# Optimization experiments

Measured on AMD Instinct MI355X. Metric: run time of the kernel, lower is better.

## Reference

```python
import jax, jax.numpy as jnp
import numpy as np

FEAT_STRIDE = 16
PRE_NMS_TOPN = 6000
POST_NMS_TOPN = 300
NMS_THRESH = 0.7
NEG = -1e9  # sentinel for suppressed scores


def generate_anchors(base_size=16, ratios=np.array([0.5, 1.0, 2.0]), scales=np.array([8.0, 16.0, 32.0])):
    ctr = (base_size - 1) / 2.0
    size = float(base_size * base_size)
    ws_r = np.round(np.sqrt(size / ratios))
    hs_r = np.round(ws_r * ratios)
    ws = (ws_r[:, None] * scales[None, :]).reshape(-1)
    hs = (hs_r[:, None] * scales[None, :]).reshape(-1)
    return np.stack([ctr - 0.5 * (ws - 1), ctr - 0.5 * (hs - 1),
                     ctr + 0.5 * (ws - 1), ctr + 0.5 * (hs - 1)], axis=1).astype(np.float32)

ANCHORS = jnp.asarray(generate_anchors())  # [A, 4]


def bbox_transform_inv(anchors, deltas):
    # anchors [N,4], deltas [B,N,4] -> [B,N,4]
    w = anchors[:, 2] - anchors[:, 0] + 1.0
    h = anchors[:, 3] - anchors[:, 1] + 1.0
    cx = anchors[:, 0] + 0.5 * w
    cy = anchors[:, 1] + 0.5 * h
    dx, dy, dw, dh = deltas[..., 0], deltas[..., 1], deltas[..., 2], deltas[..., 3]
    pcx = dx * w + cx
    pcy = dy * h + cy
    pw = jnp.exp(dw) * w
    ph = jnp.exp(dh) * h
    return jnp.stack([pcx - 0.5 * pw, pcy - 0.5 * ph, pcx + 0.5 * pw, pcy + 0.5 * ph], axis=-1)


def nms_single(boxes, scores):
    # Greedy NMS on pre-sorted candidates; boxes [N,4], scores [N].
    areas = (boxes[:, 2] - boxes[:, 0] + 1.0) * (boxes[:, 3] - boxes[:, 1] + 1.0)

    def body(sc, _):
        i = jnp.argmax(sc)
        valid = sc[i] > NEG / 2
        b = boxes[i]
        xx1 = jnp.maximum(b[0], boxes[:, 0])
        yy1 = jnp.maximum(b[1], boxes[:, 1])
        xx2 = jnp.minimum(b[2], boxes[:, 2])
        yy2 = jnp.minimum(b[3], boxes[:, 3])
        inter = jnp.maximum(xx2 - xx1 + 1.0, 0.0) * jnp.maximum(yy2 - yy1 + 1.0, 0.0)
        iou = inter / (areas[i] + areas - inter)
        sc = jnp.where(iou > NMS_THRESH, NEG, sc)  # suppress (includes self, iou=1)
        return sc, (i, valid)

    _, (keep, valid) = jax.lax.scan(body, scores, None, length=POST_NMS_TOPN)
    kept_boxes = jnp.where(valid[:, None], boxes[keep], 0.0)  # pad rows -> zeros
    return kept_boxes


def reference(scores, bbox_deltas, im_info):
    B, _, H, W = scores.shape
    A = ANCHORS.shape[0]
    # fg probs: second set of A channels -> [B, K*A]
    fg = jnp.transpose(scores[:, A:, :, :], (0, 2, 3, 1)).reshape(B, -1)
    deltas = jnp.transpose(bbox_deltas, (0, 2, 3, 1)).reshape(B, -1, 4)

    # Shifted anchors over the feature grid: [K*A, 4]
    sx = jnp.arange(W, dtype=jnp.float32) * FEAT_STRIDE
    sy = jnp.arange(H, dtype=jnp.float32) * FEAT_STRIDE
    mx, my = jnp.meshgrid(sx, sy)  # [H, W]
    shifts = jnp.stack([mx.ravel(), my.ravel(), mx.ravel(), my.ravel()], axis=1)  # [K,4]
    anchors = (ANCHORS[None, :, :] + shifts[:, None, :]).reshape(-1, 4)

    proposals = bbox_transform_inv(anchors, deltas)  # [B, K*A, 4]

    # Clip to image per batch element (im_info = [height, width, scale])
    wmax = (im_info[:, 1] - 1.0)[:, None]
    hmax = (im_info[:, 0] - 1.0)[:, None]
    proposals = jnp.stack([
        jnp.clip(proposals[..., 0], 0.0, wmax),
        jnp.clip(proposals[..., 1], 0.0, hmax),
        jnp.clip(proposals[..., 2], 0.0, wmax),
        jnp.clip(proposals[..., 3], 0.0, hmax)], axis=-1)

    # Top pre_nms_topN by score (sorted descending)
    top_scores, top_idx = jax.lax.top_k(fg, PRE_NMS_TOPN)            # [B, pre]
    top_boxes = jnp.take_along_axis(proposals, top_idx[..., None], axis=1)  # [B, pre, 4]

    kept = jax.vmap(nms_single)(top_boxes, top_scores)  # [B, post, 4]

    batch_col = jnp.broadcast_to(
        jnp.arange(B, dtype=kept.dtype)[:, None, None], (B, POST_NMS_TOPN, 1))
    return jnp.concatenate([batch_col, kept], axis=-1)  # [B, post, 5]


def setup_inputs() -> dict:
    key = jax.random.key(0)
    k1, k2 = jax.random.split(key)
    B, A, H, W = 16, 9, 192, 192
    scores = jax.random.uniform(k1, (B, 2 * A, H, W), dtype=jnp.float32)
    bbox_deltas = jax.random.normal(k2, (B, 4 * A, H, W), dtype=jnp.float32) * 0.5
    im_info = jnp.tile(jnp.array([[H * 16.0, W * 16.0, 1.0]], dtype=jnp.float32), (B, 1))
    return {"scores": scores, "bbox_deltas": bbox_deltas, "im_info": im_info}
```

## Files before the change

### kernel.cpp

```cpp
#include <hip/hip_runtime.h>
#include <stdint.h>

#define A_NUM    9
#define W_FEAT   192
#define H_FEAT   192
#define K_FEAT   (W_FEAT * H_FEAT)
#define N_ANCH   (K_FEAT * A_NUM)
#define BATCH    16
#define PRE_NMS  6000
#define POST_NMS 300
#define CAP      8192
#define CHUNK    4096
#define BPB      (N_ANCH / CHUNK)
#define CPA      (K_FEAT / CHUNK)
#define SORT2    2048
#define NWORD    (SORT2 / 64)
#define SLOTS    64

#define T2KEY    0xBF7Fu

typedef unsigned long long u64;

__constant__ float c_anchors[A_NUM][4] = {
    { -84.f,  -40.f,  99.f,  55.f},
    {-176.f,  -88.f, 191.f, 103.f},
    {-360.f, -184.f, 375.f, 199.f},
    { -56.f,  -56.f,  71.f,  71.f},
    {-120.f, -120.f, 135.f, 135.f},
    {-248.f, -248.f, 263.f, 263.f},
    { -36.f,  -80.f,  51.f,  95.f},
    { -80.f, -168.f,  95.f, 183.f},
    {-168.f, -344.f, 183.f, 359.f},
};

__device__ __forceinline__ unsigned key_bits(float s) {
    unsigned ub = __float_as_uint(s);
    return (ub & 0x80000000u) ? ~ub : (ub | 0x80000000u);
}

__device__ __forceinline__ const float* chunk_ptr(const float* scores, int blk,
                                                  int& b, int& a, int& koff) {
    b = blk / BPB;
    int chunk = blk - b * BPB;
    a = chunk / CPA;
    koff = (chunk - a * CPA) * CHUNK;
    return scores + ((size_t)(b * 2 * A_NUM + A_NUM + a)) * K_FEAT + koff;
}

__device__ __forceinline__ void hist_add(unsigned* lh, unsigned bin) {
    unsigned long long peers = __ballot(1);
    #pragma unroll
    for (int bit = 0; bit < 8; ++bit) {
        unsigned long long vote = __ballot((bin >> bit) & 1);
        peers &= ((bin >> bit) & 1) ? vote : ~vote;
    }
    int lane = threadIdx.x & 63;
    if (lane == (int)(__ffsll((long long)peers) - 1))
        atomicAdd(&lh[bin], (unsigned)__popcll(peers));
}

__device__ __forceinline__ float4 decode_box(unsigned n, const float* __restrict__ deltas,
                                             int b, float wmax, float hmax) {
    unsigned kk = n / A_NUM, a = n - kk * A_NUM;
    unsigned hh = kk / W_FEAT, ww = kk - hh * W_FEAT;
    size_t dbase = ((size_t)(b * 4 * A_NUM + 4 * a)) * K_FEAT + kk;
    float dx = deltas[dbase];
    float dy = deltas[dbase + (size_t)K_FEAT];
    float dw = deltas[dbase + (size_t)2 * K_FEAT];
    float dh = deltas[dbase + (size_t)3 * K_FEAT];
    float ax1 = c_anchors[a][0] + ww * 16.0f;
    float ay1 = c_anchors[a][1] + hh * 16.0f;
    float ax2 = c_anchors[a][2] + ww * 16.0f;
    float ay2 = c_anchors[a][3] + hh * 16.0f;
    float waf = ax2 - ax1 + 1.0f, haf = ay2 - ay1 + 1.0f;
    float cx = ax1 + 0.5f * waf, cy = ay1 + 0.5f * haf;
    float pcx = dx * waf + cx, pcy = dy * haf + cy;
    float pw = expf(dw) * waf, ph = expf(dh) * haf;
    float4 box;
    box.x = fminf(fmaxf(pcx - 0.5f * pw, 0.f), wmax);
    box.y = fminf(fmaxf(pcy - 0.5f * ph, 0.f), hmax);
    box.z = fminf(fmaxf(pcx + 0.5f * pw, 0.f), wmax);
    box.w = fminf(fmaxf(pcy + 0.5f * ph, 0.f), hmax);
    return box;
}

__device__ __forceinline__ bool iou_over(float4 a, float aa, float4 c, float ca) {
    float xx1 = fmaxf(a.x, c.x), yy1 = fmaxf(a.y, c.y);
    float xx2 = fminf(a.z, c.z), yy2 = fminf(a.w, c.w);
    float iw = fmaxf(xx2 - xx1 + 1.f, 0.f);
    float ih = fmaxf(yy2 - yy1 + 1.f, 0.f);
    float inter = iw * ih;
    return inter > 0.7f * (aa + ca - inter);
}

__device__ __forceinline__ u64 shflxor64(u64 v, int j) {
    unsigned lo = (unsigned)v, hi = (unsigned)(v >> 32);
    lo = __shfl_xor(lo, j, 64);
    hi = __shfl_xor(hi, j, 64);
    return ((u64)hi << 32) | lo;
}

__global__ __launch_bounds__(256) void compact_kernel(
        const float* __restrict__ scores,
        unsigned* __restrict__ cnt_blk,
        u64* __restrict__ cand) {
    __shared__ u64 sbuf[256];
    __shared__ unsigned scount;
    int tid = threadIdx.x;
    if (tid == 0) scount = 0;
    __syncthreads();
    int b, a, koff;
    const float* p = chunk_ptr(scores, blockIdx.x, b, a, koff);
    const float4* p4 = (const float4*)p;
    #pragma unroll
    for (int it = 0; it < CHUNK / 1024; ++it) {
        float4 v = p4[it * 256 + tid];
        unsigned e0 = (unsigned)(koff + (it * 256 + tid) * 4);
        float vv[4] = {v.x, v.y, v.z, v.w};
        #pragma unroll
        for (int j = 0; j < 4; ++j) {
            unsigned ub = key_bits(vv[j]);
            if ((ub >> 16) >= T2KEY) {
                unsigned n = (e0 + j) * A_NUM + a;
                unsigned pos = atomicAdd(&scount, 1u);
                if (pos < 256)
                    sbuf[pos] = ((u64)ub << 32) | (unsigned)(~n);
            }
        }
    }
    __syncthreads();
    unsigned c = scount;
    if (tid == 0) cnt_blk[blockIdx.x] = c;
    unsigned cw = c < SLOTS ? c : SLOTS;
    if (tid < cw) cand[(size_t)blockIdx.x * SLOTS + tid] = sbuf[tid];
}

#define KEYRD(I)  ((((u64)khi[(I)]) << 32) | klo[(I)])
#define KEYWR(I, V) do { khi[(I)] = (unsigned)((V) >> 32); klo[(I)] = (unsigned)(V); } while (0)

#define CE_SHFL(E, J, DESC) do { \
    u64 _v = shflxor64((E), (J)); \
    bool _kmax = ((DESC) == ((l & (J)) == 0)); \
    (E) = _kmax ? ((E) > _v ? (E) : _v) : ((E) < _v ? (E) : _v); \
} while (0)

#define CE_PAIR(A, B, DESC) do { \
    u64 _mx = (A) > (B) ? (A) : (B); \
    u64 _mn = (A) > (B) ? (B) : (A); \
    if (DESC) { (A) = _mx; (B) = _mn; } else { (A) = _mn; (B) = _mx; } \
} while (0)

#define LDS_PHASE(K, J) do { \
    _Pragma("unroll") \
    for (int pp = 0; pp < 2; ++pp) { \
        unsigned p = (unsigned)tid + (unsigned)pp * 512u; \
        unsigned i = ((p & ~((unsigned)(J) - 1u)) << 1) | (p & ((unsigned)(J) - 1u)); \
        unsigned ixj = i | (unsigned)(J); \
        u64 x = KEYRD(i), y = KEYRD(ixj); \
        bool dsc = ((i & (unsigned)(K)) == 0u); \
        if (dsc ? (x < y) : (x > y)) { KEYWR(i, y); KEYWR(ixj, x); } \
    } \
    __syncthreads(); \
} while (0)

#define REG_TAIL(D) do { \
    int seg = w << 8; \
    bool d = (D); \
    u64 e0 = KEYRD(seg + l); \
    u64 e1 = KEYRD(seg + 64 + l); \
    u64 e2 = KEYRD(seg + 128 + l); \
    u64 e3 = KEYRD(seg + 192 + l); \
    CE_PAIR(e0, e2, d); CE_PAIR(e1, e3, d); \
    CE_PAIR(e0, e1, d); CE_PAIR(e2, e3, d); \
    _Pragma("unroll") \
    for (int j = 32; j >= 1; j >>= 1) { \
        CE_SHFL(e0, j, d); CE_SHFL(e1, j, d); \
        CE_SHFL(e2, j, d); CE_SHFL(e3, j, d); \
    } \
    KEYWR(seg + l, e0); KEYWR(seg + 64 + l, e1); \
    KEYWR(seg + 128 + l, e2); KEYWR(seg + 192 + l, e3); \
    __syncthreads(); \
} while (0)

__global__ __launch_bounds__(512) void sort_kernel(
        const unsigned* __restrict__ cnt_blk,
        const u64* __restrict__ cand,
        const float* __restrict__ deltas,
        const float* __restrict__ im_info,
        float4* __restrict__ bxg,
        unsigned* __restrict__ m2arr,
        unsigned* __restrict__ okarr) {
    int b = blockIdx.x;
    __shared__ unsigned khi[SORT2];
    __shared__ unsigned klo[SORT2];
    __shared__ unsigned offs[BPB + 1];
    __shared__ unsigned ovfl;
    int tid = threadIdx.x;
    int l = tid & 63, w = tid >> 6;

    if (tid == 0) { ovfl = 0; offs[0] = 0; }
    __syncthreads();
    if (tid < BPB) {
        unsigned c = cnt_blk[b * BPB + tid];
        if (c > SLOTS) atomicOr(&ovfl, 1u);
        offs[tid + 1] = (c > SLOTS) ? SLOTS : c;
    }
    for (int i = tid; i < SORT2; i += 512) { khi[i] = 0u; klo[i] = 0u; }
    __syncthreads();
    if (tid == 0)
        for (int i = 1; i <= BPB; ++i) offs[i] += offs[i - 1];
    __syncthreads();
    unsigned m2 = offs[BPB];
    bool ok = (!ovfl) && (m2 >= 1) && (m2 <= SORT2);

    if (ok) {
        for (int s = w; s < BPB; s += 8) {
            unsigned c = offs[s + 1] - offs[s];
            if ((unsigned)l < c) {
                u64 k = cand[(size_t)(b * BPB + s) * SLOTS + l];
                KEYWR(offs[s] + l, k);
            }
        }
    }
    __syncthreads();

    if (ok) {
        {
            int seg = w << 8;
            u64 e0 = KEYRD(seg + l);
            u64 e1 = KEYRD(seg + 64 + l);
            u64 e2 = KEYRD(seg + 128 + l);
            u64 e3 = KEYRD(seg + 192 + l);
            #pragma unroll
            for (int k = 2; k <= 32; k <<= 1) {
                bool d = ((l & k) == 0);
                #pragma unroll
                for (int j = k >> 1; j >= 1; j >>= 1) {
                    CE_SHFL(e0, j, d); CE_SHFL(e1, j, d);
                    CE_SHFL(e2, j, d); CE_SHFL(e3, j, d);
                }
            }
            #pragma unroll
            for (int j = 32; j >= 1; j >>= 1) {
                CE_SHFL(e0, j, true);  CE_SHFL(e1, j, false);
                CE_SHFL(e2, j, true);  CE_SHFL(e3, j, false);
            }
            CE_PAIR(e0, e1, true); CE_PAIR(e2, e3, false);
            #pragma unroll
            for (int j = 32; j >= 1; j >>= 1) {
                CE_SHFL(e0, j, true);  CE_SHFL(e1, j, true);
                CE_SHFL(e2, j, false); CE_SHFL(e3, j, false);
            }
            {
                bool d = ((w & 1) == 0);
                CE_PAIR(e0, e2, d); CE_PAIR(e1, e3, d);
                CE_PAIR(e0, e1, d); CE_PAIR(e2, e3, d);
                #pragma unroll
                for (int j = 32; j >= 1; j >>= 1) {
                    CE_SHFL(e0, j, d); CE_SHFL(e1, j, d);
                    CE_SHFL(e2, j, d); CE_SHFL(e3, j, d);
                }
            }
            KEYWR(seg + l, e0); KEYWR(seg + 64 + l, e1);
            KEYWR(seg + 128 + l, e2); KEYWR(seg + 192 + l, e3);
        }
        __syncthreads();
        LDS_PHASE(512, 256);                 REG_TAIL(((w & 2) == 0));
        LDS_PHASE(1024, 512); LDS_PHASE(1024, 256);  REG_TAIL(((w & 4) == 0));
        LDS_PHASE(2048, 1024); LDS_PHASE(2048, 512); LDS_PHASE(2048, 256);
        REG_TAIL(true);

        float wmax = im_info[b * 3 + 1] - 1.0f;
        float hmax = im_info[b * 3 + 0] - 1.0f;
        int mceil = (int)((m2 + 63u) & ~63u);
        for (int i = tid; i < mceil; i += 512) {
            float4 v;
            if (i < (int)m2) v = decode_box(~klo[i], deltas, b, wmax, hmax);
            else             v = make_float4(-3e9f, -3e9f, -3e9f, -3e9f);
            bxg[(size_t)b * SORT2 + i] = v;
        }
    }
    if (tid == 0) { m2arr[b] = m2; okarr[b] = ok ? 1u : 0u; }
}

__global__ __launch_bounds__(256) void mask_kernel(
        const float4* __restrict__ bxg,
        const unsigned* __restrict__ m2arr,
        const unsigned* __restrict__ okarr,
        u64* __restrict__ mask) {
    int b = blockIdx.x >> 5;
    int t = blockIdx.x & 31;
    if (!okarr[b]) return;
    unsigned m2 = m2arr[b];
    if ((unsigned)(t * 64) >= m2) return;
    __shared__ float4 sb[SORT2];
    __shared__ float  sa[SORT2];
    int tid = threadIdx.x;
    int mceil = (int)((m2 + 63u) & ~63u);
    for (int i = tid; i < mceil; i += 256) {
        float4 v = bxg[(size_t)b * SORT2 + i];
        sb[i] = v;
        sa[i] = (v.z - v.x + 1.f) * (v.w - v.y + 1.f);
    }
    __syncthreads();
    int r = t * 64 + (tid >> 2);
    int q = tid & 3;
    float4 rb = sb[r];
    float  ra = sa[r];
    u64* mrow = mask + ((size_t)b * SORT2 + r) * NWORD;
    for (int w = t + q; w < NWORD; w += 4) {
        if (w * 64 >= mceil) break;
        u64 bits = 0;
        #pragma unroll 4
        for (int jj = 0; jj < 64; ++jj) {
            int j = w * 64 + jj;
            bits |= ((u64)(iou_over(rb, ra, sb[j], sa[j]) ? 1 : 0)) << jj;
        }
        mrow[w] = bits;
    }
}

__global__ __launch_bounds__(512) void resolve_fb_kernel(
        const float4* __restrict__ bxg,
        const u64* __restrict__ mask,
        const unsigned* __restrict__ m2arr,
        const unsigned* __restrict__ okarr,
        const float* __restrict__ scores,
        const float* __restrict__ deltas,
        const float* __restrict__ im_info,
        float4* __restrict__ fbbox,
        float* __restrict__ out) {
    int b = blockIdx.x;
    int tid = threadIdx.x;
    __shared__ unsigned short kept_idx[POST_NMS];
    __shared__ unsigned nk_sh;
    __shared__ unsigned lh[256];
    __shared__ unsigned d8_sh, above_sh, tbin_sh, fbcnt;
    __shared__ u64 keys[CAP];

    bool okb = (okarr[b] != 0);
    if (tid == 0) nk_sh = 0;
    __syncthreads();

    if (okb && tid < 64) {
        int lane = tid;
        int m2 = (int)m2arr[b];
        const u64* mb = mask + (size_t)b * SORT2 * NWORD;
        u64 S = 0;
        int w32 = lane & 31;
        bool hiHalf = lane >= 32;
        int nchunks = (m2 + 63) >> 6;
        u64 dpre = mb[(size_t)lane * NWORD + 0];
        int nk = 0;
        for (int c = 0; c < nchunks && nk < POST_NMS; ++c) {
            int base = c * 64;
            int nvalid = min(64, m2 - base);
            u64 d = dpre;
            if (c + 1 < nchunks)
                dpre = mb[(size_t)(base + 64 + lane) * NWORD + (c + 1)];
            unsigned wl0 = __builtin_amdgcn_readlane((unsigned)S, c);
            unsigned wh0 = __builtin_amdgcn_readlane((unsigned)(S >> 32), c);
            unsigned wl1 = __builtin_amdgcn_readlane((unsigned)S, c + 32);
            unsigned wh1 = __builtin_amdgcn_readlane((unsigned)(S >> 32), c + 32);
            u64 Sc = (((u64)wh0 << 32) | wl0) | (((u64)wh1 << 32) | wl1);
            u64 live = ~Sc;
            if (nvalid < 64) live &= (1ull << nvalid) - 1ull;
            u64 keptC = 0;
            while (live && nk < POST_NMS) {
                int il = (int)__ffsll((long long)live) - 1;
                unsigned dlo = __builtin_amdgcn_readlane((unsigned)d, il);
                unsigned dhi = __builtin_amdgcn_readlane((unsigned)(d >> 32), il);
                u64 drow = ((u64)dhi << 32) | dlo;
                live &= ~drow;
                live &= ~(1ull << il);
                if (lane == 0) kept_idx[nk] = (unsigned short)(base + il);
                keptC |= 1ull << il;
                ++nk;
            }
            if (nk < POST_NMS && c + 1 < nchunks && keptC) {
                long long kc = (long long)keptC;
                while (kc) {
                    int r0  = (int)__ffsll(kc) - 1; kc &= kc - 1;
                    int r1  = (int)__ffsll(kc) - 1; kc &= kc - 1;
                    int r2  = (int)__ffsll(kc) - 1; kc &= kc - 1;
                    int r3  = (int)__ffsll(kc) - 1; kc &= kc - 1;
                    int r4  = (int)__ffsll(kc) - 1; kc &= kc - 1;
                    int r5  = (int)__ffsll(kc) - 1; kc &= kc - 1;
                    int r6  = (int)__ffsll(kc) - 1; kc &= kc - 1;
                    int r7  = (int)__ffsll(kc) - 1; kc &= kc - 1;
                    int r8  = (int)__ffsll(kc) - 1; kc &= kc - 1;
                    int r9  = (int)__ffsll(kc) - 1; kc &= kc - 1;
                    int r10 = (int)__ffsll(kc) - 1; kc &= kc - 1;
                    int r11 = (int)__ffsll(kc) - 1; kc &= kc - 1;
                    int r12 = (int)__ffsll(kc) - 1; kc &= kc - 1;
                    int r13 = (int)__ffsll(kc) - 1; kc &= kc - 1;
                    int r14 = (int)__ffsll(kc) - 1; kc &= kc - 1;
                    int r15 = (int)__ffsll(kc) - 1; kc &= kc - 1;
                    int s0 = hiHalf ? r1  : r0;
                    int s1 = hiHalf ? r3  : r2;
                    int s2 = hiHalf ? r5  : r4;
                    int s3 = hiHalf ? r7  : r6;
                    int s4 = hiHalf ? r9  : r8;
                    int s5 = hiHalf ? r11 : r10;
                    int s6 = hiHalf ? r13 : r12;
                    int s7 = hiHalf ? r15 : r14;
                    u64 a0 = 0, a1 = 0, a2 = 0, a3 = 0;
                    u64 a4 = 0, a5 = 0, a6 = 0, a7 = 0;
                    if (s0 >= 0) a0 = mb[(size_t)(base + s0) * NWORD + w32];
                    if (s1 >= 0) a1 = mb[(size_t)(base + s1) * NWORD + w32];
                    if (s2 >= 0) a2 = mb[(size_t)(base + s2) * NWORD + w32];
                    if (s3 >= 0) a3 = mb[(size_t)(base + s3) * NWORD + w32];
                    if (s4 >= 0) a4 = mb[(size_t)(base + s4) * NWORD + w32];
                    if (s5 >= 0) a5 = mb[(size_t)(base + s5) * NWORD + w32];
                    if (s6 >= 0) a6 = mb[(size_t)(base + s6) * NWORD + w32];
                    if (s7 >= 0) a7 = mb[(size_t)(base + s7) * NWORD + w32];
                    S |= (a0 | a1) | (a2 | a3) | (a4 | a5) | (a6 | a7);
                }
            }
        }
        if (lane == 0) nk_sh = (unsigned)nk;
    }
    __syncthreads();

    unsigned nk = nk_sh;
    bool ok_final = okb && (nk == POST_NMS);
    if (ok_final) {
        const float4* bx = bxg + (size_t)b * SORT2;
        for (int t = tid; t < POST_NMS; t += 512) {
            float4 kb = bx[kept_idx[t]];
            float* o = out + ((size_t)b * POST_NMS + t) * 5;
            o[0] = (float)b;
            o[1] = kb.x; o[2] = kb.y; o[3] = kb.z; o[4] = kb.w;
        }
        return;
    }

    if (tid < 256) lh[tid] = 0;
    __syncthreads();
    for (int a = 0; a < A_NUM; ++a) {
        const float* p = scores + ((size_t)(b * 2 * A_NUM + A_NUM + a)) * K_FEAT;
        for (int k = tid; k < K_FEAT; k += 512)
            hist_add(lh, key_bits(p[k]) >> 24);
    }
    __syncthreads();
    if (tid == 0) {
        unsigned acc = 0; int d = 0;
        for (int i = 255; i >= 0; --i) {
            unsigned v = lh[i];
            if (acc + v >= PRE_NMS) { d = i; break; }
            acc += v;
        }
        d8_sh = (unsigned)d; above_sh = acc;
    }
    __syncthreads();
    unsigned dd = d8_sh;
    if (tid < 256) lh[tid] = 0;
    __syncthreads();
    for (int a = 0; a < A_NUM; ++a) {
        const float* p = scores + ((size_t)(b * 2 * A_NUM + A_NUM + a)) * K_FEAT;
        for (int k = tid; k < K_FEAT; k += 512) {
            unsigned u = key_bits(p[k]);
            if ((u >> 24) == dd) hist_add(lh, (u >> 16) & 0xFF);
        }
    }
    __syncthreads();
    if (tid == 0) {
        unsigned acc = above_sh; int d = 0;
        for (int i = 255; i >= 0; --i) {
            unsigned v = lh[i];
            if (acc + v >= PRE_NMS) { d = i; break; }
            acc += v;
        }
        tbin_sh = (dd << 8) | (unsigned)d;
        fbcnt = 0;
    }
    __syncthreads();
    unsigned tb = tbin_sh;
    for (int i = tid; i < CAP; i += 512) keys[i] = 0ULL;
    __syncthreads();
    for (int a = 0; a < A_NUM; ++a) {
        const float* p = scores + ((size_t)(b * 2 * A_NUM + A_NUM + a)) * K_FEAT;
        for (int k = tid; k < K_FEAT; k += 512) {
            unsigned u = key_bits(p[k]);
            if ((u >> 16) >= tb) {
                unsigned n = (unsigned)k * A_NUM + (unsigned)a;
                unsigned pos = atomicAdd(&fbcnt, 1u);
                if (pos < CAP) keys[pos] = ((u64)u << 32) | (unsigned)(~n);
            }
        }
    }
    __syncthreads();
    for (unsigned k = 2; k <= CAP; k <<= 1) {
        for (unsigned j = k >> 1; j > 0; j >>= 1) {
            #pragma unroll
            for (int pp = 0; pp < 8; ++pp) {
                unsigned p = (unsigned)tid + (unsigned)pp * 512u;
                unsigned i = ((p & ~(j - 1)) << 1) | (p & (j - 1));
                unsigned ixj = i | j;
                u64 x = keys[i], y = keys[ixj];
                bool desc = ((i & k) == 0);
                if (desc ? (x < y) : (x > y)) { keys[i] = y; keys[ixj] = x; }
            }
            __syncthreads();
        }
    }
    float wmax = im_info[b * 3 + 1] - 1.0f;
    float hmax = im_info[b * 3 + 0] - 1.0f;
    for (int i = tid; i < PRE_NMS; i += 512) {
        unsigned n = ~(unsigned)(keys[i] & 0xFFFFFFFFull);
        float4 box = make_float4(0.f, 0.f, 0.f, 0.f);
        if (n < N_ANCH) box = decode_box(n, deltas, b, wmax, hmax);
        fbbox[(size_t)b * PRE_NMS + i] = box;
    }
    __syncthreads();
    if (tid >= 64) return;
    int lane = tid;
    float4 k0, k1v, k2v, k3v, k4v;
    float a0 = 1.f, a1 = 1.f, a2 = 1.f, a3 = 1.f, a4 = 1.f;
    k0 = k1v = k2v = k3v = k4v = make_float4(0.f, 0.f, 0.f, 0.f);
    const float4* bb = fbbox + (size_t)b * PRE_NMS;
    int nk2 = 0;
    for (int i = 0; i < PRE_NMS && nk2 < POST_NMS; ++i) {
        float4 cur = bb[i];
        float ca = (cur.z - cur.x + 1.f) * (cur.w - cur.y + 1.f);
        bool s = false;
        if (nk2 > 0)   { bool v = lane < nk2;       s |= v && iou_over(k0,  a0, cur, ca); }
        if (nk2 > 64)  { bool v = 64 + lane < nk2;  s |= v && iou_over(k1v, a1, cur, ca); }
        if (nk2 > 128) { bool v = 128 + lane < nk2; s |= v && iou_over(k2v, a2, cur, ca); }
        if (nk2 > 192) { bool v = 192 + lane < nk2; s |= v && iou_over(k3v, a3, cur, ca); }
        if (nk2 > 256) { bool v = 256 + lane < nk2; s |= v && iou_over(k4v, a4, cur, ca); }
        if (!__any(s)) {
            int r = nk2 >> 6;
            if (lane == (nk2 & 63)) {
                if      (r == 0) { k0  = cur; a0 = ca; }
                else if (r == 1) { k1v = cur; a1 = ca; }
                else if (r == 2) { k2v = cur; a2 = ca; }
                else if (r == 3) { k3v = cur; a3 = ca; }
                else             { k4v = cur; a4 = ca; }
            }
            if (lane == 0) {
                float* o = out + ((size_t)b * POST_NMS + nk2) * 5;
                o[0] = (float)b;
                o[1] = cur.x; o[2] = cur.y; o[3] = cur.z; o[4] = cur.w;
            }
            ++nk2;
        }
    }
    for (int t = nk2 + lane; t < POST_NMS; t += 64) {
        float* o = out + ((size_t)b * POST_NMS + t) * 5;
        o[0] = (float)b;
        o[1] = 0.f; o[2] = 0.f; o[3] = 0.f; o[4] = 0.f;
    }
}

extern "C" void kernel_launch(void* const* d_in, const int* in_sizes, int n_in,
                              void* d_out, int out_size, void* d_ws, size_t ws_size,
                              hipStream_t stream) {
    const float* scores  = (const float*)d_in[0];
    const float* deltas  = (const float*)d_in[1];
    const float* im_info = (const float*)d_in[2];
    float* out = (float*)d_out;

    size_t off = 0;
    unsigned* cnt_blk = (unsigned*)((char*)d_ws + off);
    off += (size_t)BATCH * BPB * 4;
    off = (off + 255) & ~(size_t)255;
    u64* cand = (u64*)((char*)d_ws + off);
    off += (size_t)BATCH * BPB * SLOTS * 8;
    off = (off + 255) & ~(size_t)255;
    unsigned* m2arr = (unsigned*)((char*)d_ws + off);
    off += (size_t)BATCH * 4;
    off = (off + 255) & ~(size_t)255;
    unsigned* okarr = (unsigned*)((char*)d_ws + off);
    off += (size_t)BATCH * 4;
    off = (off + 255) & ~(size_t)255;
    float4* bxg = (float4*)((char*)d_ws + off);
    off += (size_t)BATCH * SORT2 * 16;
    off = (off + 255) & ~(size_t)255;
    u64* mask = (u64*)((char*)d_ws + off);
    off += (size_t)BATCH * SORT2 * NWORD * 8;
    off = (off + 255) & ~(size_t)255;
    float4* fbbox = (float4*)((char*)d_ws + off);

    compact_kernel   <<<BATCH * BPB, 256, 0, stream>>>(scores, cnt_blk, cand);
    sort_kernel      <<<BATCH, 512, 0, stream>>>(cnt_blk, cand, deltas, im_info,
                                                 bxg, m2arr, okarr);
    mask_kernel      <<<BATCH * 32, 256, 0, stream>>>(bxg, m2arr, okarr, mask);
    resolve_fb_kernel<<<BATCH, 512, 0, stream>>>(bxg, mask, m2arr, okarr,
                                                 scores, deltas, im_info,
                                                 fbbox, out);
}
```

Baseline: 105.9 us.

## Double-buffer NMS mask chunks in LDS with producer waves prefetching

The serial greedy NMS resolve now stages each 64-row chunk of the suppression mask in shared memory. Waves 1-7 prefetch the next chunk into a second buffer while wave 0 scans the current chunk, and all waves synchronize once per chunk. This replaces wave 0's scattered global loads of kept rows with LDS reads, aiming to hide memory latency on the serial critical path. In exchange it adds a block-wide barrier per chunk and copies whole chunks even when only a few rows are kept; the fallback sort keys now reuse the same 64KB buffer.

```diff
diff --git a/kernel.cpp b/kernel.cpp
--- a/kernel.cpp
+++ b/kernel.cpp
@@ -332,93 +332,77 @@
         float* __restrict__ out) {
     int b = blockIdx.x;
     int tid = threadIdx.x;
+    int wv = tid >> 6;
+    __shared__ __align__(16) char smem[65536];
     __shared__ unsigned short kept_idx[POST_NMS];
     __shared__ unsigned nk_sh;
     __shared__ unsigned lh[256];
     __shared__ unsigned d8_sh, above_sh, tbin_sh, fbcnt;
-    __shared__ u64 keys[CAP];
+
+    u64* rowbuf = (u64*)smem;
 
     bool okb = (okarr[b] != 0);
+    int m2 = okb ? (int)m2arr[b] : 0;
+    int nchunks = (m2 + 63) >> 6;
+    const u64* mb = mask + (size_t)b * SORT2 * NWORD;
     if (tid == 0) nk_sh = 0;
-    __syncthreads();
-
-    if (okb && tid < 64) {
-        int lane = tid;
-        int m2 = (int)m2arr[b];
-        const u64* mb = mask + (size_t)b * SORT2 * NWORD;
+
+    if (okb) {
+        for (int i = tid; i < 64 * NWORD; i += 512)
+            rowbuf[i] = mb[i];
+    }
+    __syncthreads();
+
+    if (okb) {
+        int lane = tid & 63;
+        int w32c = lane & 31;
         u64 S = 0;
-        int w32 = lane & 31;
-        bool hiHalf = lane >= 32;
-        int nchunks = (m2 + 63) >> 6;
-        u64 dpre = mb[(size_t)lane * NWORD + 0];
         int nk = 0;
-        for (int c = 0; c < nchunks && nk < POST_NMS; ++c) {
-            int base = c * 64;
-            int nvalid = min(64, m2 - base);
-            u64 d = dpre;
-            if (c + 1 < nchunks)
-                dpre = mb[(size_t)(base + 64 + lane) * NWORD + (c + 1)];
-            unsigned wl0 = __builtin_amdgcn_readlane((unsigned)S, c);
-            unsigned wh0 = __builtin_amdgcn_readlane((unsigned)(S >> 32), c);
-            unsigned wl1 = __builtin_amdgcn_readlane((unsigned)S, c + 32);
-            unsigned wh1 = __builtin_amdgcn_readlane((unsigned)(S >> 32), c + 32);
-            u64 Sc = (((u64)wh0 << 32) | wl0) | (((u64)wh1 << 32) | wl1);
-            u64 live = ~Sc;
-            if (nvalid < 64) live &= (1ull << nvalid) - 1ull;
-            u64 keptC = 0;
-            while (live && nk < POST_NMS) {
-                int il = (int)__ffsll((long long)live) - 1;
-                unsigned dlo = __builtin_amdgcn_readlane((unsigned)d, il);
-                unsigned dhi = __builtin_amdgcn_readlane((unsigned)(d >> 32), il);
-                u64 drow = ((u64)dhi << 32) | dlo;
-                live &= ~drow;
-                live &= ~(1ull << il);
-                if (lane == 0) kept_idx[nk] = (unsigned short)(base + il);
-                keptC |= 1ull << il;
-                ++nk;
-            }
-            if (nk < POST_NMS && c + 1 < nchunks && keptC) {
-                long long kc = (long long)keptC;
-                while (kc) {
-                    int r0  = (int)__ffsll(kc) - 1; kc &= kc - 1;
-                    int r1  = (int)__ffsll(kc) - 1; kc &= kc - 1;
-                    int r2  = (int)__ffsll(kc) - 1; kc &= kc - 1;
-                    int r3  = (int)__ffsll(kc) - 1; kc &= kc - 1;
-                    int r4  = (int)__ffsll(kc) - 1; kc &= kc - 1;
-                    int r5  = (int)__ffsll(kc) - 1; kc &= kc - 1;
-                    int r6  = (int)__ffsll(kc) - 1; kc &= kc - 1;
-                    int r7  = (int)__ffsll(kc) - 1; kc &= kc - 1;
-                    int r8  = (int)__ffsll(kc) - 1; kc &= kc - 1;
-                    int r9  = (int)__ffsll(kc) - 1; kc &= kc - 1;
-                    int r10 = (int)__ffsll(kc) - 1; kc &= kc - 1;
-                    int r11 = (int)__ffsll(kc) - 1; kc &= kc - 1;
-                    int r12 = (int)__ffsll(kc) - 1; kc &= kc - 1;
-                    int r13 = (int)__ffsll(kc) - 1; kc &= kc - 1;
-                    int r14 = (int)__ffsll(kc) - 1; kc &= kc - 1;
-                    int r15 = (int)__ffsll(kc) - 1; kc &= kc - 1;
-                    int s0 = hiHalf ? r1  : r0;
-                    int s1 = hiHalf ? r3  : r2;
-                    int s2 = hiHalf ? r5  : r4;
-                    int s3 = hiHalf ? r7  : r6;
-                    int s4 = hiHalf ? r9  : r8;
-                    int s5 = hiHalf ? r11 : r10;
-                    int s6 = hiHalf ? r13 : r12;
-                    int s7 = hiHalf ? r15 : r14;
-                    u64 a0 = 0, a1 = 0, a2 = 0, a3 = 0;
-                    u64 a4 = 0, a5 = 0, a6 = 0, a7 = 0;
-                    if (s0 >= 0) a0 = mb[(size_t)(base + s0) * NWORD + w32];
-                    if (s1 >= 0) a1 = mb[(size_t)(base + s1) * NWORD + w32];
-                    if (s2 >= 0) a2 = mb[(size_t)(base + s2) * NWORD + w32];
-                    if (s3 >= 0) a3 = mb[(size_t)(base + s3) * NWORD + w32];
-                    if (s4 >= 0) a4 = mb[(size_t)(base + s4) * NWORD + w32];
-                    if (s5 >= 0) a5 = mb[(size_t)(base + s5) * NWORD + w32];
-                    if (s6 >= 0) a6 = mb[(size_t)(base + s6) * NWORD + w32];
-                    if (s7 >= 0) a7 = mb[(size_t)(base + s7) * NWORD + w32];
-                    S |= (a0 | a1) | (a2 | a3) | (a4 | a5) | (a6 | a7);
+        int cur = 0;
+        for (int c = 0; c < nchunks; ++c) {
+            int nxt = cur ^ 1;
+            if (wv > 0) {
+                if (c + 1 < nchunks) {
+                    const u64* src = mb + (size_t)(c + 1) * 64 * NWORD;
+                    for (int i = tid - 64; i < 64 * NWORD; i += 448)
+                        rowbuf[nxt * (64 * NWORD) + i] = src[i];
                 }
-            }
-        }
-        if (lane == 0) nk_sh = (unsigned)nk;
+            } else if (nk < POST_NMS) {
+                int base = c * 64;
+                int nvalid = min(64, m2 - base);
+                u64* rc = rowbuf + cur * (64 * NWORD);
+                u64 d = rc[lane * NWORD + c];
+                unsigned wl0 = __builtin_amdgcn_readlane((unsigned)S, c);
+                unsigned wh0 = __builtin_amdgcn_readlane((unsigned)(S >> 32), c);
+                unsigned wl1 = __builtin_amdgcn_readlane((unsigned)S, c + 32);
+                unsigned wh1 = __builtin_amdgcn_readlane((unsigned)(S >> 32), c + 32);
+                u64 Sc = (((u64)wh0 << 32) | wl0) | (((u64)wh1 << 32) | wl1);
+                u64 live = ~Sc;
+                if (nvalid < 64) live &= (1ull << nvalid) - 1ull;
+                u64 keptC = 0;
+                while (live && nk < POST_NMS) {
+                    int il = (int)__ffsll((long long)live) - 1;
+                    unsigned dlo = __builtin_amdgcn_readlane((unsigned)d, il);
+                    unsigned dhi = __builtin_amdgcn_readlane((unsigned)(d >> 32), il);
+                    u64 drow = ((u64)dhi << 32) | dlo;
+                    live &= ~drow;
+                    live &= ~(1ull << il);
+                    if (lane == 0) kept_idx[nk] = (unsigned short)(base + il);
+                    keptC |= 1ull << il;
+                    ++nk;
+                }
+                if (nk < POST_NMS && c + 1 < nchunks) {
+                    long long kc = (long long)keptC;
+                    while (kc) {
+                        int s = (int)__ffsll(kc) - 1; kc &= kc - 1;
+                        S |= rc[s * NWORD + w32c];
+                    }
+                }
+                if (lane == 0) nk_sh = (unsigned)nk;
+            }
+            __syncthreads();
+            cur = nxt;
+        }
     }
     __syncthreads();
 
@@ -435,6 +419,8 @@
         return;
     }
 
+    u64* keys = (u64*)smem;
+    __syncthreads();
     if (tid < 256) lh[tid] = 0;
     __syncthreads();
     for (int a = 0; a < A_NUM; ++a) {
```

Result: slower. 134.8 us (+27.3%).
